# Optimization experiments

Measured on AMD Instinct MI355X. Metric: run time of the kernel, lower is better.

## Reference

```python
import jax, jax.numpy as jnp
import numpy as np

P = 8  # patch_size hard-coded in the module


def conv1x1(x, W, b):
    # x: [B,C,H,W_], W: [O,C], b: [O]  (1x1 conv == per-pixel linear)
    return jnp.einsum('oc,bchw->bohw', W, x) + b[None, :, None, None]


def to_patch_tokens(t):
    # Replicates t.unfold(2,P,P).unfold(3,P,P).contiguous().view(B,-1,N)
    # t: [B,Cq,W,H] -> [B, Cq*P*P, N] with N = (W//P)*(H//P)
    B, Cq, Wd, Hd = t.shape
    Wp, Hp = Wd // P, Hd // P
    t = t.reshape(B, Cq, Wp, P, Hp, P).transpose(0, 1, 2, 4, 3, 5)  # [B,Cq,Wp,Hp,P,P]
    return t.reshape(B, Cq * P * P, Wp * Hp)


def setup_inputs() -> dict:
    key = jax.random.key(0)
    ks = jax.random.split(key, 10)
    B, C, Wd, Hd = 8, 64, 256, 256
    Cq = C // 8
    s_in = 1.0 / np.sqrt(C)
    s_out = 1.0 / np.sqrt(Cq)
    return {
        'x': jax.random.normal(ks[0], (B, C, Wd, Hd), jnp.float32),
        'Wq': jax.random.normal(ks[1], (Cq, C), jnp.float32) * s_in,
        'bq': jax.random.normal(ks[2], (Cq,), jnp.float32) * 0.01,
        'Wk': jax.random.normal(ks[3], (Cq, C), jnp.float32) * s_in,
        'bk': jax.random.normal(ks[4], (Cq,), jnp.float32) * 0.01,
        'Wv': jax.random.normal(ks[5], (Cq, C), jnp.float32) * s_in,
        'bv': jax.random.normal(ks[6], (Cq,), jnp.float32) * 0.01,
        'Wo': jax.random.normal(ks[7], (C, Cq), jnp.float32) * s_out,
        'bo': jax.random.normal(ks[8], (C,), jnp.float32) * 0.01,
        'gamma': jax.random.normal(ks[9], (1,), jnp.float32),
    }


def reference(x, Wq, bq, Wk, bk, Wv, bv, Wo, bo, gamma):
    B, C, Wd, Hd = x.shape
    Cq = C // 8
    q = to_patch_tokens(conv1x1(x, Wq, bq)).transpose(0, 2, 1)  # [B,N,M]
    k = to_patch_tokens(conv1x1(x, Wk, bk))                     # [B,M,N]
    v = to_patch_tokens(conv1x1(x, Wv, bv))                     # [B,M,N]
    N = k.shape[-1]  # d_k in source == number of patch tokens
    energy = jnp.einsum('bnm,bmk->bnk', q, k) / jnp.sqrt(jnp.float32(N))
    attn = jax.nn.softmax(energy, axis=-1)                      # [B,N,N]
    out = jnp.einsum('bmn,bjn->bmj', v, attn)                   # bmm(v, attn^T)
    out = out.transpose(0, 2, 1).reshape(B, Cq, Wd, Hd)
    out = conv1x1(out, Wo, bo)
    return gamma * out + x
```

## Files before the change

kernel.cpp:

```cpp
#include <hip/hip_runtime.h>
#include <stdint.h>

typedef unsigned short u16;
typedef unsigned int   u32;
typedef __attribute__((ext_vector_type(8))) short  short8;
typedef __attribute__((ext_vector_type(4))) float  floatx4;

__device__ __forceinline__ u16 f32_to_bf16(float f) {
  u32 u = __builtin_bit_cast(u32, f);
  u = (u + 0x7fffu + ((u >> 16) & 1u)) >> 16;
  return (u16)u;
}
__device__ __forceinline__ float bf16_to_f32(u16 h) {
  u32 u = ((u32)h) << 16;
  return __builtin_bit_cast(float, u);
}
__device__ __forceinline__ u32 pack2(float a, float b) {
  return (u32)f32_to_bf16(a) | ((u32)f32_to_bf16(b) << 16);
}

__device__ __forceinline__ void load_lds16(const u16* g, u16* l) {
  auto gp = (const __attribute__((address_space(1))) u32*)(uintptr_t)g;
  auto lp = (__attribute__((address_space(3))) u32*)(u32)(uintptr_t)l;
  __builtin_amdgcn_global_load_lds(gp, lp, 16, 0, 0);
}

__device__ __forceinline__ int swz(int tk) { return tk ^ ((tk >> 3) & 56); }

__global__ __launch_bounds__(512) void qkv_kernel(
    const float* __restrict__ x,
    const float* __restrict__ Wq, const float* __restrict__ bq,
    const float* __restrict__ Wk, const float* __restrict__ bk,
    const float* __restrict__ Wv, const float* __restrict__ bv,
    u16* __restrict__ qt, u16* __restrict__ kt, u16* __restrict__ vm)
{
  __shared__ __align__(16) u16 qs[8 * 1024];
  __shared__ __align__(16) u16 ks_[8 * 1024];
  __shared__ __align__(16) u16 vs[8 * 1024];

  const int wg = blockIdx.x;
  const int s  = blockIdx.y;
  const int b  = blockIdx.z;
  const int t  = threadIdx.x;
  const int wrow = t >> 6;
  const int hl2  = (t & 63) * 2;
  const int w  = wg * 8 + wrow;
  const int h  = s * 128 + hl2;

  float bqr[8], bkr[8], bvr[8];
#pragma unroll
  for (int i = 0; i < 8; i++) { bqr[i] = bq[i]; bkr[i] = bk[i]; bvr[i] = bv[i]; }

  float aq[2][8], ak[2][8], av[2][8];
#pragma unroll
  for (int j = 0; j < 2; j++)
#pragma unroll
    for (int i = 0; i < 8; i++) { aq[j][i] = 0.f; ak[j][i] = 0.f; av[j][i] = 0.f; }

  const float* xp = x + (size_t)b * 64 * 65536 + w * 256 + h;
#pragma unroll 4
  for (int c = 0; c < 64; c++) {
    const float2 xv = *(const float2*)(xp + (size_t)c * 65536);
#pragma unroll
    for (int cq = 0; cq < 8; cq++) {
      const float wqv = Wq[cq * 64 + c];
      const float wkv = Wk[cq * 64 + c];
      const float wvv = Wv[cq * 64 + c];
      aq[0][cq] = fmaf(wqv, xv.x, aq[0][cq]);
      aq[1][cq] = fmaf(wqv, xv.y, aq[1][cq]);
      ak[0][cq] = fmaf(wkv, xv.x, ak[0][cq]);
      ak[1][cq] = fmaf(wkv, xv.y, ak[1][cq]);
      av[0][cq] = fmaf(wvv, xv.x, av[0][cq]);
      av[1][cq] = fmaf(wvv, xv.y, av[1][cq]);
    }
  }

  const int tk0 = ((hl2 >> 3) << 6) | (wrow << 3) | (hl2 & 7);
  const int st  = swz(tk0);
#pragma unroll
  for (int cq = 0; cq < 8; cq++) {
    *(u32*)(qs  + cq * 1024 + st) = pack2(aq[0][cq] + bqr[cq], aq[1][cq] + bqr[cq]);
    *(u32*)(ks_ + cq * 1024 + st) = pack2(ak[0][cq] + bkr[cq], ak[1][cq] + bkr[cq]);
    *(u32*)(vs  + cq * 1024 + st) = pack2(av[0][cq] + bvr[cq], av[1][cq] + bvr[cq]);
  }
  __syncthreads();

  const int wq = wg >> 2;
  const int mc = (wg & 3) * 2 + s;
  const int colbase = wq * 64 + mc * 8;

#pragma unroll
  for (int i = 0; i < 2; i++) {
    const int tk = i * 512 + t;
    const int sk = swz(tk);
    uint4 qv, kv;
    qv.x = (u32)qs[sk]        | ((u32)qs[1024 + sk] << 16);
    qv.y = (u32)qs[2048 + sk] | ((u32)qs[3072 + sk] << 16);
    qv.z = (u32)qs[4096 + sk] | ((u32)qs[5120 + sk] << 16);
    qv.w = (u32)qs[6144 + sk] | ((u32)qs[7168 + sk] << 16);
    kv.x = (u32)ks_[sk]        | ((u32)ks_[1024 + sk] << 16);
    kv.y = (u32)ks_[2048 + sk] | ((u32)ks_[3072 + sk] << 16);
    kv.z = (u32)ks_[4096 + sk] | ((u32)ks_[5120 + sk] << 16);
    kv.w = (u32)ks_[6144 + sk] | ((u32)ks_[7168 + sk] << 16);
    *(uint4*)(qt + ((size_t)b * 1024 + tk) * 512 + colbase) = qv;
    *(uint4*)(kt + ((size_t)b * 1024 + tk) * 512 + colbase) = kv;
  }

#pragma unroll
  for (int cq = 0; cq < 8; cq++) {
    const int mrow = cq * 64 + wq * 8 + mc;
    const u32 val = *(const u32*)(vs + cq * 1024 + swz(2 * t));
    *(u32*)(vm + ((size_t)b * 512 + mrow) * 1024 + 2 * t) = val;
  }
}

template <int FMW>
__global__ __launch_bounds__(512) void gemm_nt(
    const u16* __restrict__ A, const u16* __restrict__ Bm, u16* __restrict__ Cm,
    int M, int N, int K, float scale)
{
  constexpr int BM = FMW * 32;
  constexpr int NA = BM / 64;
  __shared__ __align__(16) u16 As[2][BM * 64];
  __shared__ __align__(16) u16 Bs[2][128 * 64];

  const int bz = blockIdx.x, bn = blockIdx.y, bm = blockIdx.z;
  const int t = threadIdx.x;
  const int lane = t & 63, wid = t >> 6;
  const int wm = wid & 1, wn = wid >> 1;
  const int m0 = bm * BM, n0 = bn * 128;

  const u16* Ab = A + (size_t)bz * M * K + (size_t)m0 * K;
  const u16* Bb = Bm + (size_t)bz * N * K + (size_t)n0 * K;

  floatx4 acc[FMW][2];
#pragma unroll
  for (int i = 0; i < FMW; i++)
#pragma unroll
    for (int j = 0; j < 2; j++) acc[i][j] = (floatx4){0.f, 0.f, 0.f, 0.f};

  const int srow = wid * 8 + (lane >> 3);
  const int scol = (((lane & 7) ^ ((lane >> 3) & 7)) << 3);
  const int l15 = lane & 15, quad = lane >> 4;
  const int cxor = (l15 & 7) << 3;

#pragma unroll
  for (int i = 0; i < NA; i++)
    load_lds16(Ab + (size_t)(i * 64 + srow) * K + scol, As[0] + (i * 64 + wid * 8) * 64);
#pragma unroll
  for (int i = 0; i < 2; i++)
    load_lds16(Bb + (size_t)(i * 64 + srow) * K + scol, Bs[0] + (i * 64 + wid * 8) * 64);
  __syncthreads();

  const int nk = K >> 6;
#pragma unroll 2
  for (int kk = 0; kk < nk; kk++) {
    const int cur = kk & 1;
    if (kk + 1 < nk) {
      const int k1 = (kk + 1) << 6;
#pragma unroll
      for (int i = 0; i < NA; i++)
        load_lds16(Ab + (size_t)(i * 64 + srow) * K + k1 + scol,
                   As[cur ^ 1] + (i * 64 + wid * 8) * 64);
#pragma unroll
      for (int i = 0; i < 2; i++)
        load_lds16(Bb + (size_t)(i * 64 + srow) * K + k1 + scol,
                   Bs[cur ^ 1] + (i * 64 + wid * 8) * 64);
    }
#pragma unroll
    for (int ks = 0; ks < 2; ks++) {
      const int koff = (ks * 32 + quad * 8) ^ cxor;
      short8 a[FMW], b[2];
#pragma unroll
      for (int f = 0; f < FMW; f++)
        a[f] = *(const short8*)(As[cur] + (wm * FMW * 16 + f * 16 + l15) * 64 + koff);
#pragma unroll
      for (int f = 0; f < 2; f++)
        b[f] = *(const short8*)(Bs[cur] + (wn * 32 + f * 16 + l15) * 64 + koff);
#pragma unroll
      for (int fm = 0; fm < FMW; fm++)
#pragma unroll
        for (int fn = 0; fn < 2; fn++)
          acc[fm][fn] = __builtin_amdgcn_mfma_f32_16x16x32_bf16(a[fm], b[fn], acc[fm][fn], 0, 0, 0);
    }
    __syncthreads();
  }

  u16* Cb = Cm + (size_t)bz * M * N;
#pragma unroll
  for (int fm = 0; fm < FMW; fm++)
#pragma unroll
    for (int fn = 0; fn < 2; fn++)
#pragma unroll
      for (int r = 0; r < 4; r++) {
        int row = m0 + wm * FMW * 16 + fm * 16 + quad * 4 + r;
        int col = n0 + wn * 32 + fn * 16 + l15;
        Cb[(size_t)row * N + col] = f32_to_bf16(scale * acc[fm][fn][r]);
      }
}

__global__ __launch_bounds__(256) void softmax_kernel(u16* __restrict__ EP)
{
  const int r = (blockIdx.x << 2) + (threadIdx.x >> 6);
  const int lane = threadIdx.x & 63;
  u16* row = EP + (size_t)r * 1024;
  const uint4* rp = (const uint4*)row;

  uint4 v0 = rp[lane * 2];
  uint4 v1 = rp[lane * 2 + 1];
  const u32 wds[8] = {v0.x, v0.y, v0.z, v0.w, v1.x, v1.y, v1.z, v1.w};
  float e[16];
#pragma unroll
  for (int i = 0; i < 8; i++) {
    e[2 * i]     = bf16_to_f32((u16)wds[i]);
    e[2 * i + 1] = bf16_to_f32((u16)(wds[i] >> 16));
  }

  float mx = e[0];
#pragma unroll
  for (int i = 1; i < 16; i++) mx = fmaxf(mx, e[i]);
#pragma unroll
  for (int off = 32; off > 0; off >>= 1) mx = fmaxf(mx, __shfl_xor(mx, off));

  float s = 0.f;
#pragma unroll
  for (int i = 0; i < 16; i++) { e[i] = __expf(e[i] - mx); s += e[i]; }
#pragma unroll
  for (int off = 32; off > 0; off >>= 1) s += __shfl_xor(s, off);

  const float inv = 1.0f / s;
  uint4 o0, o1;
  o0.x = pack2(e[0] * inv,  e[1] * inv);
  o0.y = pack2(e[2] * inv,  e[3] * inv);
  o0.z = pack2(e[4] * inv,  e[5] * inv);
  o0.w = pack2(e[6] * inv,  e[7] * inv);
  o1.x = pack2(e[8] * inv,  e[9] * inv);
  o1.y = pack2(e[10] * inv, e[11] * inv);
  o1.z = pack2(e[12] * inv, e[13] * inv);
  o1.w = pack2(e[14] * inv, e[15] * inv);
  ((uint4*)row)[lane * 2]     = o0;
  ((uint4*)row)[lane * 2 + 1] = o1;
}

__global__ __launch_bounds__(256) void out_kernel(
    const float* __restrict__ x, const u16* __restrict__ OT,
    const float* __restrict__ Wo, const float* __restrict__ bo,
    const float* __restrict__ gammap, float* __restrict__ out)
{
  const int gb = blockIdx.x;
  const int osel = gb & 1;
  const int q2 = (gb >> 1) * 256 + threadIdx.x;
  const int b = q2 >> 15;
  const int rem = (q2 & 32767) * 2;
  const float gmv = gammap[0];

  const u16* otb = OT + (size_t)b * 524288;
  const int m0 = rem & 511;
  const int nbase = rem >> 9;
  float oc[8][2];
#pragma unroll
  for (int cq = 0; cq < 8; cq++) {
    ushort2 hv = *(const ushort2*)(otb + (size_t)(cq * 128 + nbase) * 512 + m0);
    oc[cq][0] = bf16_to_f32(hv.x);
    oc[cq][1] = bf16_to_f32(hv.y);
  }

  const size_t obase = (size_t)b * 4194304 + rem + (size_t)osel * 32 * 65536;
  const float* xb = x + obase;
  float* ob = out + obase;
  const int o0 = osel * 32;
#pragma unroll 4
  for (int oo = 0; oo < 32; oo++) {
    const int o = o0 + oo;
    const float2 xv = *(const float2*)(xb + (size_t)oo * 65536);
    const float bv = bo[o];
    float a0 = bv, a1 = bv;
#pragma unroll
    for (int cq = 0; cq < 8; cq++) {
      const float wv = Wo[o * 8 + cq];
      a0 = fmaf(wv, oc[cq][0], a0);
      a1 = fmaf(wv, oc[cq][1], a1);
    }
    float2 rv;
    rv.x = fmaf(gmv, a0, xv.x);
    rv.y = fmaf(gmv, a1, xv.y);
    *(float2*)(ob + (size_t)oo * 65536) = rv;
  }
}

extern "C" void kernel_launch(void* const* d_in, const int* in_sizes, int n_in,
                              void* d_out, int out_size, void* d_ws, size_t ws_size,
                              hipStream_t stream) {
  const float* x  = (const float*)d_in[0];
  const float* Wq = (const float*)d_in[1];
  const float* bq = (const float*)d_in[2];
  const float* Wk = (const float*)d_in[3];
  const float* bk = (const float*)d_in[4];
  const float* Wv = (const float*)d_in[5];
  const float* bv = (const float*)d_in[6];
  const float* Wo = (const float*)d_in[7];
  const float* bo = (const float*)d_in[8];
  const float* gm = (const float*)d_in[9];
  float* out = (float*)d_out;

  u16* qt = (u16*)d_ws;
  u16* kt = qt + 4194304;
  u16* vm = kt + 4194304;
  u16* EP = vm + 4194304;
  u16* OT = qt;

  qkv_kernel<<<dim3(32, 2, 8), 512, 0, stream>>>(x, Wq, bq, Wk, bk, Wv, bv, qt, kt, vm);
  gemm_nt<4><<<dim3(8, 8, 8), 512, 0, stream>>>(qt, kt, EP, 1024, 1024, 512, 0.03125f);
  softmax_kernel<<<2048, 256, 0, stream>>>(EP);
  gemm_nt<2><<<dim3(8, 4, 16), 512, 0, stream>>>(EP, vm, OT, 1024, 512, 1024, 1.0f);
  out_kernel<<<2048, 256, 0, stream>>>(x, OT, Wo, bo, gm, out);
}
```

Before: 323.4 us.

## Halve GEMM N-tile to 64 and software-prefetch x channels in QKV projection

```diff
diff --git a/kernel.cpp b/kernel.cpp
--- a/kernel.cpp
+++ b/kernel.cpp
@@ -58,21 +58,38 @@
     for (int i = 0; i < 8; i++) { aq[j][i] = 0.f; ak[j][i] = 0.f; av[j][i] = 0.f; }
 
   const float* xp = x + (size_t)b * 64 * 65536 + w * 256 + h;
-#pragma unroll 4
-  for (int c = 0; c < 64; c++) {
-    const float2 xv = *(const float2*)(xp + (size_t)c * 65536);
-#pragma unroll
-    for (int cq = 0; cq < 8; cq++) {
-      const float wqv = Wq[cq * 64 + c];
-      const float wkv = Wk[cq * 64 + c];
-      const float wvv = Wv[cq * 64 + c];
-      aq[0][cq] = fmaf(wqv, xv.x, aq[0][cq]);
-      aq[1][cq] = fmaf(wqv, xv.y, aq[1][cq]);
-      ak[0][cq] = fmaf(wkv, xv.x, ak[0][cq]);
-      ak[1][cq] = fmaf(wkv, xv.y, ak[1][cq]);
-      av[0][cq] = fmaf(wvv, xv.x, av[0][cq]);
-      av[1][cq] = fmaf(wvv, xv.y, av[1][cq]);
-    }
+
+  float2 xr[8];
+#pragma unroll
+  for (int i = 0; i < 8; i++) xr[i] = *(const float2*)(xp + (size_t)i * 65536);
+
+#pragma unroll
+  for (int c0 = 0; c0 < 64; c0 += 8) {
+    float2 xn[8];
+    if (c0 + 8 < 64) {
+#pragma unroll
+      for (int i = 0; i < 8; i++)
+        xn[i] = *(const float2*)(xp + (size_t)(c0 + 8 + i) * 65536);
+    }
+#pragma unroll
+    for (int i = 0; i < 8; i++) {
+      const int c = c0 + i;
+      const float2 xv = xr[i];
+#pragma unroll
+      for (int cq = 0; cq < 8; cq++) {
+        const float wqv = Wq[cq * 64 + c];
+        const float wkv = Wk[cq * 64 + c];
+        const float wvv = Wv[cq * 64 + c];
+        aq[0][cq] = fmaf(wqv, xv.x, aq[0][cq]);
+        aq[1][cq] = fmaf(wqv, xv.y, aq[1][cq]);
+        ak[0][cq] = fmaf(wkv, xv.x, ak[0][cq]);
+        ak[1][cq] = fmaf(wkv, xv.y, ak[1][cq]);
+        av[0][cq] = fmaf(wvv, xv.x, av[0][cq]);
+        av[1][cq] = fmaf(wvv, xv.y, av[1][cq]);
+      }
+    }
+#pragma unroll
+    for (int i = 0; i < 8; i++) xr[i] = xn[i];
   }
 
   const int tk0 = ((hl2 >> 3) << 6) | (wrow << 3) | (hl2 & 7);
@@ -122,22 +139,20 @@
   constexpr int BM = FMW * 32;
   constexpr int NA = BM / 64;
   __shared__ __align__(16) u16 As[2][BM * 64];
-  __shared__ __align__(16) u16 Bs[2][128 * 64];
+  __shared__ __align__(16) u16 Bs[2][64 * 64];
 
   const int bz = blockIdx.x, bn = blockIdx.y, bm = blockIdx.z;
   const int t = threadIdx.x;
   const int lane = t & 63, wid = t >> 6;
   const int wm = wid & 1, wn = wid >> 1;
-  const int m0 = bm * BM, n0 = bn * 128;
+  const int m0 = bm * BM, n0 = bn * 64;
 
   const u16* Ab = A + (size_t)bz * M * K + (size_t)m0 * K;
   const u16* Bb = Bm + (size_t)bz * N * K + (size_t)n0 * K;
 
-  floatx4 acc[FMW][2];
-#pragma unroll
-  for (int i = 0; i < FMW; i++)
-#pragma unroll
-    for (int j = 0; j < 2; j++) acc[i][j] = (floatx4){0.f, 0.f, 0.f, 0.f};
+  floatx4 acc[FMW];
+#pragma unroll
+  for (int i = 0; i < FMW; i++) acc[i] = (floatx4){0.f, 0.f, 0.f, 0.f};
 
   const int srow = wid * 8 + (lane >> 3);
   const int scol = (((lane & 7) ^ ((lane >> 3) & 7)) << 3);
@@ -147,9 +162,7 @@
 #pragma unroll
   for (int i = 0; i < NA; i++)
     load_lds16(Ab + (size_t)(i * 64 + srow) * K + scol, As[0] + (i * 64 + wid * 8) * 64);
-#pragma unroll
-  for (int i = 0; i < 2; i++)
-    load_lds16(Bb + (size_t)(i * 64 + srow) * K + scol, Bs[0] + (i * 64 + wid * 8) * 64);
+  load_lds16(Bb + (size_t)srow * K + scol, Bs[0] + (wid * 8) * 64);
   __syncthreads();
 
   const int nk = K >> 6;
@@ -162,26 +175,19 @@
       for (int i = 0; i < NA; i++)
         load_lds16(Ab + (size_t)(i * 64 + srow) * K + k1 + scol,
                    As[cur ^ 1] + (i * 64 + wid * 8) * 64);
-#pragma unroll
-      for (int i = 0; i < 2; i++)
-        load_lds16(Bb + (size_t)(i * 64 + srow) * K + k1 + scol,
-                   Bs[cur ^ 1] + (i * 64 + wid * 8) * 64);
+      load_lds16(Bb + (size_t)srow * K + k1 + scol, Bs[cur ^ 1] + (wid * 8) * 64);
     }
 #pragma unroll
     for (int ks = 0; ks < 2; ks++) {
       const int koff = (ks * 32 + quad * 8) ^ cxor;
-      short8 a[FMW], b[2];
+      short8 a[FMW], bfr;
 #pragma unroll
       for (int f = 0; f < FMW; f++)
         a[f] = *(const short8*)(As[cur] + (wm * FMW * 16 + f * 16 + l15) * 64 + koff);
-#pragma unroll
-      for (int f = 0; f < 2; f++)
-        b[f] = *(const short8*)(Bs[cur] + (wn * 32 + f * 16 + l15) * 64 + koff);
+      bfr = *(const short8*)(Bs[cur] + (wn * 16 + l15) * 64 + koff);
 #pragma unroll
       for (int fm = 0; fm < FMW; fm++)
-#pragma unroll
-        for (int fn = 0; fn < 2; fn++)
-          acc[fm][fn] = __builtin_amdgcn_mfma_f32_16x16x32_bf16(a[fm], b[fn], acc[fm][fn], 0, 0, 0);
+        acc[fm] = __builtin_amdgcn_mfma_f32_16x16x32_bf16(a[fm], bfr, acc[fm], 0, 0, 0);
     }
     __syncthreads();
   }
@@ -190,13 +196,11 @@
 #pragma unroll
   for (int fm = 0; fm < FMW; fm++)
 #pragma unroll
-    for (int fn = 0; fn < 2; fn++)
-#pragma unroll
-      for (int r = 0; r < 4; r++) {
-        int row = m0 + wm * FMW * 16 + fm * 16 + quad * 4 + r;
-        int col = n0 + wn * 32 + fn * 16 + l15;
-        Cb[(size_t)row * N + col] = f32_to_bf16(scale * acc[fm][fn][r]);
-      }
+    for (int r = 0; r < 4; r++) {
+      int row = m0 + wm * FMW * 16 + fm * 16 + quad * 4 + r;
+      int col = n0 + wn * 16 + l15;
+      Cb[(size_t)row * N + col] = f32_to_bf16(scale * acc[fm][r]);
+    }
 }
 
 __global__ __launch_bounds__(256) void softmax_kernel(u16* __restrict__ EP)
@@ -310,8 +314,8 @@
   u16* OT = qt;
 
   qkv_kernel<<<dim3(32, 2, 8), 512, 0, stream>>>(x, Wq, bq, Wk, bk, Wv, bv, qt, kt, vm);
-  gemm_nt<4><<<dim3(8, 8, 8), 512, 0, stream>>>(qt, kt, EP, 1024, 1024, 512, 0.03125f);
+  gemm_nt<4><<<dim3(8, 16, 8), 512, 0, stream>>>(qt, kt, EP, 1024, 1024, 512, 0.03125f);
   softmax_kernel<<<2048, 256, 0, stream>>>(EP);
-  gemm_nt<2><<<dim3(8, 4, 16), 512, 0, stream>>>(EP, vm, OT, 1024, 512, 1024, 1.0f);
+  gemm_nt<2><<<dim3(8, 8, 16), 512, 0, stream>>>(EP, vm, OT, 1024, 512, 1024, 1.0f);
   out_kernel<<<2048, 256, 0, stream>>>(x, OT, Wo, bo, gm, out);
 }
```

Result: slower. 345.2 us (+6.7%).

## Fuse softmax into the attention-times-V GEMM, dropping the standalone softmax pass

Applied to the files above, without the earlier changes.

```diff
diff --git a/kernel.cpp b/kernel.cpp
--- a/kernel.cpp
+++ b/kernel.cpp
@@ -23,6 +23,19 @@
   auto gp = (const __attribute__((address_space(1))) u32*)(uintptr_t)g;
   auto lp = (__attribute__((address_space(3))) u32*)(u32)(uintptr_t)l;
   __builtin_amdgcn_global_load_lds(gp, lp, 16, 0, 0);
+}
+
+__device__ __forceinline__ short8 exp_bf16x8(short8 a) {
+  short8 r;
+#pragma unroll
+  for (int i = 0; i < 4; i++) {
+    const float lo = __expf(bf16_to_f32((u16)(short)a[2 * i]));
+    const float hi = __expf(bf16_to_f32((u16)(short)a[2 * i + 1]));
+    const u32 p = pack2(lo, hi);
+    r[2 * i]     = (short)(u16)p;
+    r[2 * i + 1] = (short)(u16)(p >> 16);
+  }
+  return r;
 }
 
 __device__ __forceinline__ int swz(int tk) { return tk ^ ((tk >> 3) & 56); }
@@ -114,7 +127,7 @@
   }
 }
 
-template <int FMW>
+template <int FMW, bool SMAX>
 __global__ __launch_bounds__(512) void gemm_nt(
     const u16* __restrict__ A, const u16* __restrict__ Bm, u16* __restrict__ Cm,
     int M, int N, int K, float scale)
@@ -123,6 +136,7 @@
   constexpr int NA = BM / 64;
   __shared__ __align__(16) u16 As[2][BM * 64];
   __shared__ __align__(16) u16 Bs[2][128 * 64];
+  __shared__ float invs[64];
 
   const int bz = blockIdx.x, bn = blockIdx.y, bm = blockIdx.z;
   const int t = threadIdx.x;
@@ -132,6 +146,26 @@
 
   const u16* Ab = A + (size_t)bz * M * K + (size_t)m0 * K;
   const u16* Bb = Bm + (size_t)bz * N * K + (size_t)n0 * K;
+
+  if constexpr (SMAX) {
+    const int row = t >> 3, seg = t & 7;
+    const u16* Ar = Ab + (size_t)row * K;
+    float sum = 0.f;
+#pragma unroll 4
+    for (int i = 0; i < 16; i++) {
+      const uint4 v = *(const uint4*)(Ar + i * 64 + seg * 8);
+      const u32 wd[4] = {v.x, v.y, v.z, v.w};
+#pragma unroll
+      for (int j = 0; j < 4; j++) {
+        sum += __expf(bf16_to_f32((u16)wd[j]));
+        sum += __expf(bf16_to_f32((u16)(wd[j] >> 16)));
+      }
+    }
+    sum += __shfl_xor(sum, 1);
+    sum += __shfl_xor(sum, 2);
+    sum += __shfl_xor(sum, 4);
+    if (seg == 0) invs[row] = 1.0f / sum;
+  }
 
   floatx4 acc[FMW][2];
 #pragma unroll
@@ -172,8 +206,10 @@
       const int koff = (ks * 32 + quad * 8) ^ cxor;
       short8 a[FMW], b[2];
 #pragma unroll
-      for (int f = 0; f < FMW; f++)
+      for (int f = 0; f < FMW; f++) {
         a[f] = *(const short8*)(As[cur] + (wm * FMW * 16 + f * 16 + l15) * 64 + koff);
+        if constexpr (SMAX) a[f] = exp_bf16x8(a[f]);
+      }
 #pragma unroll
       for (int f = 0; f < 2; f++)
         b[f] = *(const short8*)(Bs[cur] + (wn * 32 + f * 16 + l15) * 64 + koff);
@@ -193,53 +229,12 @@
     for (int fn = 0; fn < 2; fn++)
 #pragma unroll
       for (int r = 0; r < 4; r++) {
-        int row = m0 + wm * FMW * 16 + fm * 16 + quad * 4 + r;
+        const int lrow = wm * FMW * 16 + fm * 16 + quad * 4 + r;
+        const float sc = SMAX ? scale * invs[lrow] : scale;
+        int row = m0 + lrow;
         int col = n0 + wn * 32 + fn * 16 + l15;
-        Cb[(size_t)row * N + col] = f32_to_bf16(scale * acc[fm][fn][r]);
+        Cb[(size_t)row * N + col] = f32_to_bf16(sc * acc[fm][fn][r]);
       }
-}
-
-__global__ __launch_bounds__(256) void softmax_kernel(u16* __restrict__ EP)
-{
-  const int r = (blockIdx.x << 2) + (threadIdx.x >> 6);
-  const int lane = threadIdx.x & 63;
-  u16* row = EP + (size_t)r * 1024;
-  const uint4* rp = (const uint4*)row;
-
-  uint4 v0 = rp[lane * 2];
-  uint4 v1 = rp[lane * 2 + 1];
-  const u32 wds[8] = {v0.x, v0.y, v0.z, v0.w, v1.x, v1.y, v1.z, v1.w};
-  float e[16];
-#pragma unroll
-  for (int i = 0; i < 8; i++) {
-    e[2 * i]     = bf16_to_f32((u16)wds[i]);
-    e[2 * i + 1] = bf16_to_f32((u16)(wds[i] >> 16));
-  }
-
-  float mx = e[0];
-#pragma unroll
-  for (int i = 1; i < 16; i++) mx = fmaxf(mx, e[i]);
-#pragma unroll
-  for (int off = 32; off > 0; off >>= 1) mx = fmaxf(mx, __shfl_xor(mx, off));
-
-  float s = 0.f;
-#pragma unroll
-  for (int i = 0; i < 16; i++) { e[i] = __expf(e[i] - mx); s += e[i]; }
-#pragma unroll
-  for (int off = 32; off > 0; off >>= 1) s += __shfl_xor(s, off);
-
-  const float inv = 1.0f / s;
-  uint4 o0, o1;
-  o0.x = pack2(e[0] * inv,  e[1] * inv);
-  o0.y = pack2(e[2] * inv,  e[3] * inv);
-  o0.z = pack2(e[4] * inv,  e[5] * inv);
-  o0.w = pack2(e[6] * inv,  e[7] * inv);
-  o1.x = pack2(e[8] * inv,  e[9] * inv);
-  o1.y = pack2(e[10] * inv, e[11] * inv);
-  o1.z = pack2(e[12] * inv, e[13] * inv);
-  o1.w = pack2(e[14] * inv, e[15] * inv);
-  ((uint4*)row)[lane * 2]     = o0;
-  ((uint4*)row)[lane * 2 + 1] = o1;
 }
 
 __global__ __launch_bounds__(256) void out_kernel(
@@ -310,8 +305,7 @@
   u16* OT = qt;
 
   qkv_kernel<<<dim3(32, 2, 8), 512, 0, stream>>>(x, Wq, bq, Wk, bk, Wv, bv, qt, kt, vm);
-  gemm_nt<4><<<dim3(8, 8, 8), 512, 0, stream>>>(qt, kt, EP, 1024, 1024, 512, 0.03125f);
-  softmax_kernel<<<2048, 256, 0, stream>>>(EP);
-  gemm_nt<2><<<dim3(8, 4, 16), 512, 0, stream>>>(EP, vm, OT, 1024, 512, 1024, 1.0f);
+  gemm_nt<4, false><<<dim3(8, 8, 8), 512, 0, stream>>>(qt, kt, EP, 1024, 1024, 512, 0.03125f);
+  gemm_nt<2, true><<<dim3(8, 4, 16), 512, 0, stream>>>(EP, vm, OT, 1024, 512, 1024, 1.0f);
   out_kernel<<<2048, 256, 0, stream>>>(x, OT, Wo, bo, gm, out);
 }
```

After: 342.7 us. 6.0% more time.
